# Kernel tuning notes

Hardware: AMD Instinct MI355X
Metric: run time of the kernel (lower is better)

## Reference

```python
import numpy as np
import jax
import jax.numpy as jnp
from collections import deque

NUM_CLASSES = 32
N_PARENTS = 4
N_CHILD = 7
SINK_WEIGHT = 0.1
EPS = 1e-7
B, D, H, W = 2, 96, 96, 96

# ---- static tree construction (mirrors adjacency_matrix / bitpack_tree / reachability) ----

def _build_adjacency():
    n = NUM_CLASSES + 1  # node 0 is the virtual root
    A = np.zeros((n, n), dtype=np.int64)
    for p in range(N_PARENTS):
        A[0, 1 + p] = 1
        for c in range(N_CHILD):
            A[1 + p, 1 + N_PARENTS + p * N_CHILD + c] = 1
    return A

ADJ = _build_adjacency()

def _reachability(A):
    # R[i, j] = 1 iff j is reachable from i (i is ancestor-or-self of j)
    R = np.eye(A.shape[0], dtype=bool) | (A > 0)
    for _ in range(A.shape[0]):
        Rn = R | (R @ (A > 0))
        if (Rn == R).all():
            break
        R = Rn
    return R

def _bitpack(A):
    # each node's bitmask encodes its path from the root; (x & group) == class tests descendant-ness
    n = A.shape[0]
    bc = np.zeros(n, dtype=np.int64)
    bg = np.zeros(n, dtype=np.int64)
    bit = 0
    q = deque([0])
    while q:
        p = q.popleft()
        ch = np.nonzero(A[p])[0]
        if len(ch) == 0:
            continue
        w = int(np.ceil(np.log2(len(ch) + 1)))
        for i, c in enumerate(ch):
            bc[c] = bc[p] | ((i + 1) << bit)
            bg[c] = bg[p] | (((1 << w) - 1) << bit)
            q.append(c)
        bit += w
    return bc, bg

_BC, _BG = _bitpack(ADJ)
BM_CLASS = _BC[1:].astype(np.int32)
BM_GROUP = _BG[1:].astype(np.int32)
RMT = _reachability(ADJ)[1:, 1:].T.astype(np.float32)  # RMT[label, c] = c is ancestor-or-self
LEAF = np.nonzero(ADJ[1:, 1:].sum(axis=1) == 0)[0].astype(np.int32)
_SIB = ((ADJ.T @ ADJ) > 0)[1:, 1:]
SINK_IDS = [N_PARENTS + p * N_CHILD for p in range(N_PARENTS)]
PARENT_OF = {s: int(ADJ[1:, 1:][:, s].argmax()) for s in SINK_IDS}
SIBS = {}
for _s in SINK_IDS:
    _row = _SIB[_s].copy()
    _row[_s] = False
    SIBS[_s] = np.nonzero(_row)[0].tolist()
# DDESC[l, c] = 1 iff class l is a descendant-or-self of class c (bitmask test)
DDESC = ((BM_CLASS[:, None] & BM_GROUP[None, :]) == BM_CLASS[None, :]).astype(np.float32)


def setup_inputs() -> dict:
    key = jax.random.key(0)
    k1, k2 = jax.random.split(key)
    images = jax.random.normal(k1, (B, NUM_CLASSES, D, H, W), dtype=jnp.float32)
    targets = jax.random.randint(k2, (B, D, H, W), 0, NUM_CLASSES, dtype=jnp.int32)
    masks = jnp.ones((B, NUM_CLASSES), dtype=bool)
    return {"images": images, "targets": targets, "masks": masks}


def reference(images, targets, masks):
    C = NUM_CLASSES
    probs = jax.nn.softmax(images, axis=1)  # activation_fn over class dim
    leaf = jnp.asarray(LEAF)
    pred = leaf[jnp.argmax(probs[:, LEAF], axis=1)]  # _argmax_leaves -> [B,D,H,W] int32
    bm_class = jnp.asarray(BM_CLASS)
    rmt = jnp.asarray(RMT)
    ddesc = jnp.asarray(DDESC)

    def per_sample(p, pr, y, m):
        p = p.reshape(C, -1).T          # [N, C] probabilities
        y = y.reshape(-1)
        pr = pr.reshape(-1)
        valid = y != 255
        vw = valid.astype(p.dtype)
        y_safe = jnp.where(valid, y, 0).astype(jnp.int32)
        mf = m.astype(p.dtype)

        # ---- sink dice (hierarchical sink/sibling logic) ----
        pred_bm = bm_class[pr]
        sds, fls = [], []
        for s in SINK_IDS:
            sib_mask = jnp.zeros_like(valid)
            for sib in SIBS[s]:
                sib_mask = sib_mask | (y_safe == sib) | ((~m[sib]) & (pr == sib))
            par = PARENT_OF[s]
            pmask = (pred_bm & int(BM_GROUP[par])) == int(BM_CLASS[par])
            tgt = (pmask & (~sib_mask)).astype(p.dtype) * vw
            pp = p[:, s] * vw
            inter = jnp.sum(pp * tgt)
            d = 1.0 - (2.0 * inter + 1e-5) / (jnp.sum(pp) + jnp.sum(tgt) + 1e-5)
            sds.append(d)
            fls.append((jnp.sum(sib_mask & valid) > 0).astype(p.dtype))
        sd = jnp.stack(sds)
        fl = jnp.stack(fls)
        cnt = fl.sum()
        sink_dice = SINK_WEIGHT * jnp.where(cnt > 0, jnp.sum(sd * fl) / jnp.maximum(cnt, 1.0), 0.0)

        # ---- main dice (smooth_nr=0) + hierarchical CE over masked classes ----
        t = rmt[y_safe]                 # [N, C] multi-hot (label + ancestors)
        wcol = vw[:, None]
        inter = jnp.sum(p * t * wcol, axis=0)
        denom = jnp.sum(p * wcol, axis=0) + jnp.sum(t * wcol, axis=0)
        dice_c = 1.0 - (2.0 * inter) / (denom + 1e-5)
        dice = jnp.sum(dice_c * mf) / jnp.maximum(mf.sum(), 1.0)

        logp = jnp.log(jnp.clip(p, EPS, 1.0 - EPS))
        ce = jnp.sum(-jnp.sum(t * logp * mf[None, :], axis=1) * vw) / jnp.maximum(vw.sum(), 1.0)

        # ---- confusion matrix via joint (pred, true) histogram + descendant matrix ----
        flat = pr.astype(jnp.int32) * C + y_safe
        hist = jnp.zeros((C * C,), p.dtype).at[flat].add(vw).reshape(C, C)  # [pred, true]
        tp = jnp.einsum('lc,lt,tc->c', ddesc, hist, ddesc)
        fp = jnp.einsum('lc,lt->c', ddesc, hist) - tp
        fn = jnp.einsum('lt,tc->c', hist, ddesc) - tp
        cm = jnp.stack([tp, fp, fn], axis=-1) * mf[:, None]
        return jnp.stack([ce, dice, sink_dice]), cm

    loss, cm = jax.vmap(per_sample)(probs, pred, targets, masks)
    return loss, cm, pred
```

## Files before the change

### kernel.cpp

```cpp
#include <hip/hip_runtime.h>

#define NC 32
#define NVOX (96*96*96)
#define NPAIR (NVOX/2)
#define NB 384
#define TPB 256

#define WS_CE     0
#define WS_SP     32
#define WS_SPT    64
#define WS_SINKI  96
#define WS_SIB    100
#define WS_TGT    104
#define WS_HIST   128
#define SLOT_STRIDE 1152
#define NSLOT     (2 * NB)
#define FINAL_OFF (NSLOT * SLOT_STRIDE)
#define CTR_IDX   124
#define NCHUNK    8
#define BLK_PER_CH (NB / NCHUNK)
#define RED_BLK_X ((2 * SLOT_STRIDE + TPB - 1) / TPB)
#define RED_NBLK  (RED_BLK_X * NCHUNK)

__device__ __forceinline__ float wave_reduce(float v) {
    #pragma unroll
    for (int off = 32; off > 0; off >>= 1)
        v += __shfl_down(v, off, 64);
    return v;
}

__global__ __launch_bounds__(TPB, 3) void voxel_kernel(
    const float* __restrict__ images,
    const int*   __restrict__ targets,
    const int*   __restrict__ masks,
    float* __restrict__ ws,
    float* __restrict__ pred_out)
{
    const int slot = blockIdx.x;
    const int b    = slot & 1;
    const int blk  = slot >> 1;
    const int tid  = threadIdx.x;

    __shared__ float s_hist[NC * NC];
    __shared__ float s_spt[NC];
    __shared__ float s_mf[NC];
    __shared__ float s_red[45];

    for (int i = tid; i < NC * NC; i += TPB) s_hist[i] = 0.f;
    if (tid < 45) s_red[tid] = 0.f;
    if (tid < NC) {
        s_spt[tid] = 0.f;
        s_mf[tid]  = (masks[b * NC + tid] != 0) ? 1.f : 0.f;
    }
    if (slot == 0) {
        float* wsf = ws + FINAL_OFF;
        for (int i = tid; i < 2 * SLOT_STRIDE; i += TPB) wsf[i] = 0.f;
        if (tid == 0) *(unsigned int*)(ws + CTR_IDX) = 0u;
    }
    __syncthreads();

    const float2* img2 = (const float2*)(images + (size_t)b * NC * NVOX);
    const int2*   tgt2 = (const int2*)(targets + (size_t)b * NVOX);
    float2*       pout2 = (float2*)(pred_out + (size_t)b * NVOX);
    float*        wsb  = ws + (size_t)slot * SLOT_STRIDE;

    float sp[NC];
    #pragma unroll
    for (int c = 0; c < NC; ++c) sp[c] = 0.f;
    float ce = 0.f;
    float sinkI[4] = {0.f, 0.f, 0.f, 0.f};
    float sibc[4]  = {0.f, 0.f, 0.f, 0.f};
    float tgtc[4]  = {0.f, 0.f, 0.f, 0.f};

    for (int vp = blk * TPB + tid; vp < NPAIR; vp += NB * TPB) {
        const int2 y2 = tgt2[vp];

        const bool validA = (y2.x != 255);
        const bool validB = (y2.y != 255);
        const int  ysA = validA ? y2.x : 0;
        const int  ysB = validB ? y2.y : 0;
        const float vwA = validA ? 1.f : 0.f;
        const float vwB = validB ? 1.f : 0.f;
        const int  pyA = (ysA >= 4) ? (ysA - 4) / 7 : -1;
        const int  pyB = (ysB >= 4) ? (ysB - 4) / 7 : -1;
        const int  pyiA = (pyA >= 0) ? pyA : 0;
        const int  pyiB = (pyB >= 0) ? pyB : 0;

        float eva[NC], evb[NC];
        float sumA = 0.f, sumB = 0.f;
        float bestA = -3.4e38f, bestB = -3.4e38f;
        float pyvA = 0.f, pyvB = 0.f, ppvA = 0.f, ppvB = 0.f;
        int   predA = 4, predB = 4;
        #pragma unroll
        for (int c = 0; c < NC; ++c) {
            const float2 x2 = img2[(size_t)c * NPAIR + vp];
            const float ea = __expf(x2.x);
            const float eb = __expf(x2.y);
            eva[c] = ea;  evb[c] = eb;
            sumA += ea;   sumB += eb;
            pyvA = (c == ysA) ? ea : pyvA;
            pyvB = (c == ysB) ? eb : pyvB;
            if (c < 4) {
                ppvA = (c == pyiA) ? ea : ppvA;
                ppvB = (c == pyiB) ? eb : ppvB;
            }
            if (c >= 4) {
                const bool gA = (x2.x > bestA);
                bestA = gA ? x2.x : bestA;
                predA = gA ? c : predA;
                const bool gB = (x2.y > bestB);
                bestB = gB ? x2.y : bestB;
                predB = gB ? c : predB;
            }
        }
        const float rinvA = 1.f / sumA;
        const float rinvB = 1.f / sumB;
        float2 pw; pw.x = (float)predA; pw.y = (float)predB;
        pout2[vp] = pw;

        const int ppA = (predA - 4) / 7;
        const int ppB = (predB - 4) / 7;
        const float eskA = (ppA == 0) ? eva[4] : (ppA == 1) ? eva[11]
                         : (ppA == 2) ? eva[18] : eva[25];
        const float eskB = (ppB == 0) ? evb[4] : (ppB == 1) ? evb[11]
                         : (ppB == 2) ? evb[18] : evb[25];

        const float pA  = pyvA * rinvA, pB  = pyvB * rinvB;
        const float qA  = ppvA * rinvA, qB  = ppvB * rinvB;
        const float skA = eskA * rinvA, skB = eskB * rinvB;

        float termA = __logf(fminf(fmaxf(pA, 1e-7f), 1.f - 1e-7f)) * s_mf[ysA];
        if (pyA >= 0)
            termA += __logf(fminf(fmaxf(qA, 1e-7f), 1.f - 1e-7f)) * s_mf[pyiA];
        float termB = __logf(fminf(fmaxf(pB, 1e-7f), 1.f - 1e-7f)) * s_mf[ysB];
        if (pyB >= 0)
            termB += __logf(fminf(fmaxf(qB, 1e-7f), 1.f - 1e-7f)) * s_mf[pyiB];
        ce -= termA * vwA + termB * vwB;

        atomicAdd(&s_spt[ysA], pA * vwA);
        if (pyA >= 0) atomicAdd(&s_spt[pyiA], qA * vwA);
        atomicAdd(&s_spt[ysB], pB * vwB);
        if (pyB >= 0) atomicAdd(&s_spt[pyiB], qB * vwB);

        atomicAdd(&s_hist[predA * NC + ysA], vwA);
        atomicAdd(&s_hist[predB * NC + ysB], vwB);

        const bool pmA = (s_mf[predA] == 0.f);
        const bool pmB = (s_mf[predB] == 0.f);
        #pragma unroll
        for (int k = 0; k < 4; ++k) {
            const int sk = 4 + 7 * k;
            {
                const bool ysib = (pyA == k) && (ysA != sk);
                const bool msib = pmA && (ppA == k) && (predA != sk);
                const bool sib  = ysib || msib;
                if (sib && validA) sibc[k] += 1.f;
                if ((ppA == k) && !sib && validA) { tgtc[k] += 1.f; sinkI[k] += skA; }
            }
            {
                const bool ysib = (pyB == k) && (ysB != sk);
                const bool msib = pmB && (ppB == k) && (predB != sk);
                const bool sib  = ysib || msib;
                if (sib && validB) sibc[k] += 1.f;
                if ((ppB == k) && !sib && validB) { tgtc[k] += 1.f; sinkI[k] += skB; }
            }
        }

        const float rwA = rinvA * vwA;
        const float rwB = rinvB * vwB;
        #pragma unroll
        for (int c = 0; c < NC; ++c)
            sp[c] = __builtin_fmaf(evb[c], rwB, __builtin_fmaf(eva[c], rwA, sp[c]));
    }

    const int lane = tid & 63;
    {
        float r = wave_reduce(ce);
        if (lane == 0) atomicAdd(&s_red[0], r);
    }
    #pragma unroll
    for (int c = 0; c < NC; ++c) {
        float r = wave_reduce(sp[c]);
        if (lane == 0) atomicAdd(&s_red[1 + c], r);
    }
    #pragma unroll
    for (int k = 0; k < 4; ++k) {
        float r = wave_reduce(sinkI[k]);
        if (lane == 0) atomicAdd(&s_red[33 + k], r);
        r = wave_reduce(sibc[k]);
        if (lane == 0) atomicAdd(&s_red[37 + k], r);
        r = wave_reduce(tgtc[k]);
        if (lane == 0) atomicAdd(&s_red[41 + k], r);
    }
    __syncthreads();

    for (int i = tid; i < NC * NC; i += TPB) wsb[WS_HIST + i] = s_hist[i];
    if (tid == 0) wsb[WS_CE] = s_red[0];
    if (tid < NC) {
        wsb[WS_SP  + tid] = s_red[1 + tid];
        wsb[WS_SPT + tid] = s_spt[tid];
    }
    if (tid < 4) {
        wsb[WS_SINKI + tid] = s_red[33 + tid];
        wsb[WS_SIB   + tid] = s_red[37 + tid];
        wsb[WS_TGT   + tid] = s_red[41 + tid];
    }
}

__global__ __launch_bounds__(TPB) void reduce_kernel(
    const float* __restrict__ ws,
    float* __restrict__ wsf,
    const int* __restrict__ masks,
    float* __restrict__ out,
    unsigned int* __restrict__ ctr)
{
    const int v = blockIdx.x * TPB + threadIdx.x;
    {
        const int b    = v / SLOT_STRIDE;
        const int val  = v % SLOT_STRIDE;
        const int blk0 = blockIdx.y * BLK_PER_CH;
        const float* base = ws + (size_t)b * SLOT_STRIDE + val;
        float s = 0.f;
        #pragma unroll 8
        for (int i = 0; i < BLK_PER_CH; ++i)
            s += base[(size_t)(2 * (blk0 + i)) * SLOT_STRIDE];
        atomicAdd(&wsf[v], s);
    }

    __shared__ unsigned int s_last;
    __threadfence();
    __syncthreads();
    if (threadIdx.x == 0) s_last = atomicAdd(ctr, 1u);
    __syncthreads();
    if (s_last != RED_NBLK - 1) return;
    __threadfence();

    __shared__ float f_col[2][NC], f_row[2][NC], f_dice[2][NC], f_mf[2][NC];
    const int t  = threadIdx.x & 63;
    const int fb = threadIdx.x >> 6;
    const bool act = (fb < 2) && (t < NC);

    if (act) {
        const float* hist = wsf + (size_t)fb * SLOT_STRIDE + WS_HIST;
        float cs = 0.f, rs = 0.f;
        for (int j = 0; j < NC; ++j) {
            cs += hist[j * NC + t];
            rs += hist[t * NC + j];
        }
        f_col[fb][t] = cs;
        f_row[fb][t] = rs;
        f_mf[fb][t]  = (masks[fb * NC + t] != 0) ? 1.f : 0.f;
    }
    __syncthreads();

    if (act) {
        const float* wsb  = wsf + (size_t)fb * SLOT_STRIDE;
        const float* hist = wsb + WS_HIST;
        const int c = t;
        float ycnt, pcnt, tp;
        if (c < 4) {
            int idx[8];
            idx[0] = c;
            for (int j = 0; j < 7; ++j) idx[1 + j] = 4 + 7 * c + j;
            ycnt = f_col[fb][c]; pcnt = f_row[fb][c];
            for (int j = 0; j < 7; ++j) { ycnt += f_col[fb][idx[1 + j]]; pcnt += f_row[fb][idx[1 + j]]; }
            tp = 0.f;
            for (int a = 0; a < 8; ++a)
                for (int d = 0; d < 8; ++d)
                    tp += hist[idx[a] * NC + idx[d]];
        } else {
            ycnt = f_col[fb][c]; pcnt = f_row[fb][c];
            tp = hist[c * NC + c];
        }
        const float mf = f_mf[fb][c];
        out[6 + (fb * NC + c) * 3 + 0] = tp * mf;
        out[6 + (fb * NC + c) * 3 + 1] = (pcnt - tp) * mf;
        out[6 + (fb * NC + c) * 3 + 2] = (ycnt - tp) * mf;
        f_dice[fb][c] = (1.f - 2.f * wsb[WS_SPT + c] / (wsb[WS_SP + c] + ycnt + 1e-5f)) * mf;
    }
    __syncthreads();

    if (fb < 2 && t == 0) {
        const float* wsb = wsf + (size_t)fb * SLOT_STRIDE;
        float vw = 0.f, dsum = 0.f, msum = 0.f;
        for (int c = 0; c < NC; ++c) {
            vw   += f_col[fb][c];
            dsum += f_dice[fb][c];
            msum += f_mf[fb][c];
        }
        const float cel  = wsb[WS_CE] / fmaxf(vw, 1.f);
        const float dice = dsum / fmaxf(msum, 1.f);
        float cnt = 0.f, sd = 0.f;
        for (int k = 0; k < 4; ++k) {
            float fl = (wsb[WS_SIB + k] > 0.f) ? 1.f : 0.f;
            float d  = 1.f - (2.f * wsb[WS_SINKI + k] + 1e-5f) /
                             (wsb[WS_SP + 4 + 7 * k] + wsb[WS_TGT + k] + 1e-5f);
            cnt += fl;
            sd  += d * fl;
        }
        out[fb * 3 + 0] = cel;
        out[fb * 3 + 1] = dice;
        out[fb * 3 + 2] = (cnt > 0.f) ? 0.1f * (sd / fmaxf(cnt, 1.f)) : 0.f;
    }
}

extern "C" void kernel_launch(void* const* d_in, const int* in_sizes, int n_in,
                              void* d_out, int out_size, void* d_ws, size_t ws_size,
                              hipStream_t stream) {
    const float* images  = (const float*)d_in[0];
    const int*   targets = (const int*)d_in[1];
    const int*   masks   = (const int*)d_in[2];
    float* out = (float*)d_out;
    float* ws  = (float*)d_ws;
    float* wsf = ws + FINAL_OFF;

    voxel_kernel<<<dim3(NSLOT), dim3(TPB), 0, stream>>>(
        images, targets, masks, ws, out + 6 + 2 * NC * 3);
    reduce_kernel<<<dim3(RED_BLK_X, NCHUNK), dim3(TPB), 0, stream>>>(
        ws, wsf, masks, out, (unsigned int*)(ws + CTR_IDX));
}
```

Measured before the change: 345.2 us.

## Software-pipeline voxel loads with register double buffering and fewer blocks

Prefetches the next iteration's 32 logit pairs and targets into registers while the current voxel pair is processed, so memory latency overlaps with the exp/argmax/accumulation work. Grid shrinks from 384 to 256 blocks per sample with a fixed trip count of 6 or 7 iterations, and launch bounds drop to 2 blocks per CU to leave room for the doubled register footprint. Risks are lower occupancy and register spilling from holding two 32-element float2 buffers, plus the hardcoded iteration split must exactly cover NPAIR.

```diff
diff --git a/kernel.cpp b/kernel.cpp
--- a/kernel.cpp
+++ b/kernel.cpp
@@ -3,8 +3,10 @@
 #define NC 32
 #define NVOX (96*96*96)
 #define NPAIR (NVOX/2)
-#define NB 384
+#define NB 256
 #define TPB 256
+#define STRIDE (NB * TPB)
+#define FULL_BLKS 192
 
 #define WS_CE     0
 #define WS_SP     32
@@ -29,7 +31,7 @@
     return v;
 }
 
-__global__ __launch_bounds__(TPB, 3) void voxel_kernel(
+__global__ __launch_bounds__(TPB, 2) void voxel_kernel(
     const float* __restrict__ images,
     const int*   __restrict__ targets,
     const int*   __restrict__ masks,
@@ -72,8 +74,25 @@
     float sibc[4]  = {0.f, 0.f, 0.f, 0.f};
     float tgtc[4]  = {0.f, 0.f, 0.f, 0.f};
 
-    for (int vp = blk * TPB + tid; vp < NPAIR; vp += NB * TPB) {
-        const int2 y2 = tgt2[vp];
+    const int iters = (blk < FULL_BLKS) ? 7 : 6;
+    int vp = blk * TPB + tid;
+
+    float2 cur[NC];
+    #pragma unroll
+    for (int c = 0; c < NC; ++c) cur[c] = img2[(size_t)c * NPAIR + vp];
+    int2 y2 = tgt2[vp];
+
+    for (int it = 0; it < iters; ++it) {
+        const bool more = (it + 1 < iters);
+        const int  vpn  = vp + STRIDE;
+
+        float2 nxt[NC];
+        int2   y2n;
+        if (more) {
+            #pragma unroll
+            for (int c = 0; c < NC; ++c) nxt[c] = img2[(size_t)c * NPAIR + vpn];
+            y2n = tgt2[vpn];
+        }
 
         const bool validA = (y2.x != 255);
         const bool validB = (y2.y != 255);
@@ -93,9 +112,10 @@
         int   predA = 4, predB = 4;
         #pragma unroll
         for (int c = 0; c < NC; ++c) {
-            const float2 x2 = img2[(size_t)c * NPAIR + vp];
-            const float ea = __expf(x2.x);
-            const float eb = __expf(x2.y);
+            const float xa = cur[c].x;
+            const float xb = cur[c].y;
+            const float ea = __expf(xa);
+            const float eb = __expf(xb);
             eva[c] = ea;  evb[c] = eb;
             sumA += ea;   sumB += eb;
             pyvA = (c == ysA) ? ea : pyvA;
@@ -105,11 +125,11 @@
                 ppvB = (c == pyiB) ? eb : ppvB;
             }
             if (c >= 4) {
-                const bool gA = (x2.x > bestA);
-                bestA = gA ? x2.x : bestA;
+                const bool gA = (xa > bestA);
+                bestA = gA ? xa : bestA;
                 predA = gA ? c : predA;
-                const bool gB = (x2.y > bestB);
-                bestB = gB ? x2.y : bestB;
+                const bool gB = (xb > bestB);
+                bestB = gB ? xb : bestB;
                 predB = gB ? c : predB;
             }
         }
@@ -171,6 +191,13 @@
         #pragma unroll
         for (int c = 0; c < NC; ++c)
             sp[c] = __builtin_fmaf(evb[c], rwB, __builtin_fmaf(eva[c], rwA, sp[c]));
+
+        if (more) {
+            #pragma unroll
+            for (int c = 0; c < NC; ++c) cur[c] = nxt[c];
+            y2 = y2n;
+            vp = vpn;
+        }
     }
 
     const int lane = tid & 63;
```

Measured after the change: 341.9 us, median of 2. No clear change (-1.0%).
